# Kernel optimization log

Hardware: AMD Instinct MI355X
Metric: run time of the kernel (lower is better)

Reference implementation:

```python
import jax, jax.numpy as jnp
import numpy as np

N_ATOMS = 50000
N_EDGES = 1_600_000
N_MOL = 500
HIDDEN = 128
FILTERS = 128
GAUSS = 50
LAYERS = 3
CUTOFF = 10.0
LOG2 = 0.6931471805599453


def ssp(x):
    # ShiftedSoftplus: softplus(x) - log(2)
    return jax.nn.softplus(x) - LOG2


def setup_inputs() -> dict:
    key = jax.random.key(0)
    ks = jax.random.split(key, 24)
    z = jax.random.randint(ks[0], (N_ATOMS,), 0, 100)
    pos = jax.random.uniform(ks[1], (N_ATOMS, 3), jnp.float32) * 5.0  # box keeps d < cutoff
    batch = jnp.sort(jax.random.randint(ks[2], (N_ATOMS,), 0, N_MOL))
    row = jax.random.randint(ks[3], (N_EDGES,), 0, N_ATOMS)
    off = jax.random.randint(ks[4], (N_EDGES,), 1, N_ATOMS)
    col = (row + off) % N_ATOMS  # guarantees row != col (no zero distances)
    edge_index = jnp.stack([row, col])
    def lin(k, fi, fo):
        return jax.random.normal(k, (fi, fo), jnp.float32) * (1.0 / np.sqrt(fi))
    emb = jax.random.normal(ks[5], (100, HIDDEN), jnp.float32)
    mlp1_w = jnp.stack([lin(jax.random.fold_in(ks[6], i), GAUSS, FILTERS) for i in range(LAYERS)])
    mlp1_b = jnp.zeros((LAYERS, FILTERS), jnp.float32)
    mlp2_w = jnp.stack([lin(jax.random.fold_in(ks[7], i), FILTERS, FILTERS) for i in range(LAYERS)])
    mlp2_b = jnp.zeros((LAYERS, FILTERS), jnp.float32)
    lin1_w = jnp.stack([lin(jax.random.fold_in(ks[8], i), HIDDEN, FILTERS) for i in range(LAYERS)])
    lin2_w = jnp.stack([lin(jax.random.fold_in(ks[9], i), FILTERS, HIDDEN) for i in range(LAYERS)])
    lin2_b = jnp.zeros((LAYERS, HIDDEN), jnp.float32)
    int_w = jnp.stack([lin(jax.random.fold_in(ks[10], i), HIDDEN, HIDDEN) for i in range(LAYERS)])
    int_b = jnp.zeros((LAYERS, HIDDEN), jnp.float32)
    out1_w = lin(ks[11], HIDDEN, HIDDEN // 2)
    out1_b = jnp.zeros((HIDDEN // 2,), jnp.float32)
    out2_w = lin(ks[12], HIDDEN // 2, 1)
    out2_b = jnp.zeros((1,), jnp.float32)
    return {"z": z, "pos": pos, "batch": batch, "edge_index": edge_index,
            "emb": emb, "mlp1_w": mlp1_w, "mlp1_b": mlp1_b, "mlp2_w": mlp2_w, "mlp2_b": mlp2_b,
            "lin1_w": lin1_w, "lin2_w": lin2_w, "lin2_b": lin2_b, "int_w": int_w, "int_b": int_b,
            "out1_w": out1_w, "out1_b": out1_b, "out2_w": out2_w, "out2_b": out2_b}


def reference(z, pos, batch, edge_index, emb, mlp1_w, mlp1_b, mlp2_w, mlp2_b,
              lin1_w, lin2_w, lin2_b, int_w, int_b, out1_w, out1_b, out2_w, out2_b):
    row, col = edge_index[0], edge_index[1]  # source j, target i
    d = jnp.linalg.norm(pos[row] - pos[col], axis=-1)  # [E]
    # GaussianSmearing
    offset = jnp.linspace(0.0, CUTOFF, GAUSS)
    coeff = -0.5 / (offset[1] - offset[0]) ** 2
    rbf = jnp.exp(coeff * (d[:, None] - offset[None, :]) ** 2)  # [E, GAUSS]
    # cosine cutoff
    C = 0.5 * (jnp.cos(d * jnp.pi / CUTOFF) + 1.0)  # [E]
    h = emb[z]  # [N, H]
    for l in range(LAYERS):
        W = ssp(rbf @ mlp1_w[l] + mlp1_b[l]) @ mlp2_w[l] + mlp2_b[l]  # [E, F]
        W = W * C[:, None]
        x = h @ lin1_w[l]                 # [N, F]
        msg = x[row] * W                  # gather from source, per-edge filter
        agg = jax.ops.segment_sum(msg, col, num_segments=N_ATOMS)  # scatter-add to targets
        x = agg @ lin2_w[l] + lin2_b[l]
        x = ssp(x)
        x = x @ int_w[l] + int_b[l]
        h = h + x                         # residual
    h = ssp(h @ out1_w + out1_b)
    h = h @ out2_w + out2_b               # [N, 1] per-atom energy
    out = jax.ops.segment_sum(h[:, 0], batch, num_segments=N_MOL)  # 'add' readout
    return out.reshape(-1)
```

## Files before the change

kernel.cpp:

```cpp
#include <hip/hip_runtime.h>
#include <math.h>

#define HID 128
#define NGAUSS 50
#define TBL 2048
#define TBL2 8192
#define DMAX 8.6605f
#define LDX 136

typedef _Float16 h4 __attribute__((ext_vector_type(4)));
typedef _Float16 f16x8 __attribute__((ext_vector_type(8)));
typedef float f32x4 __attribute__((ext_vector_type(4)));

__device__ __forceinline__ float sspf(float x) {
  float ax = fabsf(x);
  return fmaxf(x, 0.0f) + log1pf(expf(-ax)) - 0.69314718055994530942f;
}

__global__ __launch_bounds__(128) void build_table_k(
    const float* __restrict__ w1, const float* __restrict__ b1,
    const float* __restrict__ w2, const float* __restrict__ b2,
    float* __restrict__ tab) {
  int l = blockIdx.x >> 11;
  int ti = blockIdx.x & (TBL - 1);
  int j = threadIdx.x;
  __shared__ float rbf[NGAUSS];
  __shared__ float v1[HID];
  const float step = DMAX / (float)(TBL - 1);
  float d = ti * step;
  if (j < NGAUSS) {
    const float gstep = 10.0f / 49.0f;
    const float gcoeff = -12.005f;
    float diff = d - j * gstep;
    rbf[j] = expf(gcoeff * diff * diff);
  }
  __syncthreads();
  float s = b1[l * HID + j];
  const float* w1p = w1 + l * NGAUSS * HID + j;
  for (int g = 0; g < NGAUSS; g++) s = fmaf(rbf[g], w1p[g * HID], s);
  v1[j] = sspf(s);
  __syncthreads();
  float s2 = b2[l * HID + j];
  const float* w2p = w2 + l * HID * HID + j;
  for (int k = 0; k < HID; k++) s2 = fmaf(v1[k], w2p[k * HID], s2);
  float C = 0.5f * (cosf(d * 0.3141592653589793f) + 1.0f);
  tab[((size_t)l * TBL + ti) * HID + j] = s2 * C;
}

__global__ __launch_bounds__(256) void upsample_k(
    const float* __restrict__ tab, _Float16* __restrict__ tabh) {
  int idx = blockIdx.x * 256 + threadIdx.x;
  if (idx >= 3 * TBL2 * HID) return;
  int ch = idx & 127;
  int i = (idx >> 7) & (TBL2 - 1);
  int l = idx >> 20;
  float t = (float)i * ((float)(TBL - 1) / (float)(TBL2 - 1));
  int i0 = min((int)t, TBL - 2);
  float f = t - (float)i0;
  const float* base = tab + ((size_t)l * TBL + i0) * HID + ch;
  tabh[idx] = (_Float16)fmaf(f, base[HID] - base[0], base[0]);
}

__global__ __launch_bounds__(256) void wtrans10_k(
    const float* __restrict__ lin1, const float* __restrict__ lin2,
    const float* __restrict__ intw, const float* __restrict__ out1w,
    _Float16* __restrict__ out) {
  int b = blockIdx.x;
  __shared__ _Float16 tile[128 * 130];
  int t = threadIdx.x;
  if (b < 9) {
    const float* src = (b < 3 ? lin1 : (b < 6 ? lin2 : intw)) + (size_t)(b % 3) * HID * HID;
    _Float16* dst = out + (size_t)b * HID * HID;
    for (int i = t; i < HID * HID; i += 256) tile[(i >> 7) * 130 + (i & 127)] = (_Float16)src[i];
    __syncthreads();
    for (int i = t; i < HID * HID; i += 256) dst[i] = tile[(i & 127) * 130 + (i >> 7)];
  } else {
    _Float16* dst = out + (size_t)9 * HID * HID;
    for (int i = t; i < 128 * 64; i += 256) tile[(i >> 6) * 66 + (i & 63)] = (_Float16)out1w[i];
    __syncthreads();
    for (int i = t; i < 64 * 128; i += 256) dst[i] = tile[(i & 127) * 66 + (i >> 7)];
  }
}

__global__ __launch_bounds__(256) void bcount_k(
    const int* __restrict__ col, int* __restrict__ bcount, int E, int nbuck) {
  __shared__ int hist[1024];
  int t = threadIdx.x;
  int e0 = blockIdx.x * 2048;
  for (int j = t; j < nbuck; j += 256) hist[j] = 0;
  __syncthreads();
#pragma unroll
  for (int u = 0; u < 8; u++) {
    int e = e0 + u * 256 + t;
    if (e < E) atomicAdd(&hist[col[e] >> 6], 1);
  }
  __syncthreads();
  for (int j = t; j < nbuck; j += 256)
    if (hist[j]) atomicAdd(&bcount[j], hist[j]);
}

__global__ __launch_bounds__(256) void bucket_scan_k(
    const int* __restrict__ bcount, int* __restrict__ bstart,
    int* __restrict__ bcur, int nbuck, int* __restrict__ starts, int N) {
  __shared__ int sh[256];
  int t = threadIdx.x;
  int chunk = (nbuck + 255) / 256;
  int b0 = t * chunk;
  int c[8];
  int s = 0;
  for (int j = 0; j < chunk; j++) {
    int idx = b0 + j;
    int v = (idx < nbuck) ? bcount[idx] : 0;
    c[j] = v;
    s += v;
  }
  sh[t] = s;
  __syncthreads();
  for (int o = 1; o < 256; o <<= 1) {
    int v = (t >= o) ? sh[t - o] : 0;
    __syncthreads();
    sh[t] += v;
    __syncthreads();
  }
  int p = (t == 0) ? 0 : sh[t - 1];
  for (int j = 0; j < chunk; j++) {
    int idx = b0 + j;
    if (idx < nbuck) {
      bstart[idx] = p;
      bcur[idx] = p;
      p += c[j];
    }
  }
  if (t == 255) {
    bstart[nbuck] = p;
    starts[N] = p;
  }
}

__global__ __launch_bounds__(256) void scatterA_k(
    const int* __restrict__ row, const int* __restrict__ col,
    const float* __restrict__ pos, int* __restrict__ bcur,
    unsigned long long* __restrict__ tmp, int E, int nbuck) {
  __shared__ int hist[1024];
  __shared__ int base[1024];
  int t = threadIdx.x;
  int e0 = blockIdx.x * 2048;
  for (int j = t; j < nbuck; j += 256) hist[j] = 0;
  __syncthreads();
  int bkt[8];
  int rnk[8];
  unsigned long long key[8];
#pragma unroll
  for (int u = 0; u < 8; u++) {
    int e = e0 + u * 256 + t;
    bkt[u] = -1;
    if (e < E) {
      int r = row[e], c = col[e];
      float dx = pos[r * 3 + 0] - pos[c * 3 + 0];
      float dy = pos[r * 3 + 1] - pos[c * 3 + 1];
      float dz = pos[r * 3 + 2] - pos[c * 3 + 2];
      float d = sqrtf(dx * dx + dy * dy + dz * dz);
      const float inv2 = (float)(TBL2 - 1) / DMAX;
      int q = min((int)(d * inv2 + 0.5f), TBL2 - 1);
      unsigned int pay = ((unsigned int)r << 13) | (unsigned int)q;
      key[u] = ((unsigned long long)pay << 6) | (unsigned long long)(c & 63);
      bkt[u] = c >> 6;
      rnk[u] = atomicAdd(&hist[bkt[u]], 1);
    }
  }
  __syncthreads();
  for (int j = t; j < nbuck; j += 256)
    base[j] = hist[j] ? atomicAdd(&bcur[j], hist[j]) : 0;
  __syncthreads();
#pragma unroll
  for (int u = 0; u < 8; u++)
    if (bkt[u] >= 0) tmp[(size_t)base[bkt[u]] + rnk[u]] = key[u];
}

__global__ __launch_bounds__(256) void scatterB_k(
    const unsigned long long* __restrict__ tmp, const int* __restrict__ bstart,
    int* __restrict__ starts, unsigned int* __restrict__ payload, int N) {
  int j = blockIdx.x;
  int t = threadIdx.x;
  __shared__ int cnt[64];
  __shared__ int cur[64];
  int rs = bstart[j], re = bstart[j + 1];
  if (t < 64) cnt[t] = 0;
  __syncthreads();
  for (int e = rs + t; e < re; e += 256)
    atomicAdd(&cnt[(int)(tmp[e] & 63)], 1);
  __syncthreads();
  if (t < 64) {
    int mine = cnt[t];
    int v = mine;
    for (int o = 1; o < 64; o <<= 1) {
      int u = __shfl_up(v, o, 64);
      if (t >= o) v += u;
    }
    int excl = v - mine;
    int c = j * 64 + t;
    if (c < N) starts[c] = rs + excl;
    cur[t] = rs + excl;
  }
  __syncthreads();
  for (int e = rs + t; e < re; e += 256) {
    unsigned long long k = tmp[e];
    int p = atomicAdd(&cur[(int)(k & 63)], 1);
    payload[p] = (unsigned int)(k >> 6);
  }
}

__global__ __launch_bounds__(256) void lin1_emb_k(
    const int* __restrict__ z, const float* __restrict__ emb,
    const _Float16* __restrict__ W1t, float* __restrict__ h,
    _Float16* __restrict__ x16, int N) {
  int t = threadIdx.x;
  int lane = t & 63, w = t >> 6;
  int mrow = lane & 15, quad = lane >> 4;
  int a0 = blockIdx.x * 64;
  int am = a0 + w * 16 + mrow;
  int amc = min(am, N - 1);
  int zz = z[amc];
  const float* er = emb + (size_t)zz * HID;
  f16x8 af[4];
#pragma unroll
  for (int kk = 0; kk < 4; kk++) {
    float4 e0 = *(const float4*)(er + kk * 32 + quad * 8);
    float4 e1 = *(const float4*)(er + kk * 32 + quad * 8 + 4);
    if (am < N) {
      *(float4*)(h + (size_t)am * HID + kk * 32 + quad * 8) = e0;
      *(float4*)(h + (size_t)am * HID + kk * 32 + quad * 8 + 4) = e1;
    }
    f16x8 a8;
    a8[0] = (_Float16)e0.x; a8[1] = (_Float16)e0.y;
    a8[2] = (_Float16)e0.z; a8[3] = (_Float16)e0.w;
    a8[4] = (_Float16)e1.x; a8[5] = (_Float16)e1.y;
    a8[6] = (_Float16)e1.z; a8[7] = (_Float16)e1.w;
    af[kk] = a8;
  }
  f32x4 zero = {0.f, 0.f, 0.f, 0.f};
  f32x4 acc[8];
#pragma unroll
  for (int i = 0; i < 8; i++) acc[i] = zero;
#pragma unroll
  for (int kk = 0; kk < 4; kk++) {
    f16x8 bf[8];
#pragma unroll
    for (int nt = 0; nt < 8; nt++)
      bf[nt] = *(const f16x8*)(W1t + (size_t)(nt * 16 + mrow) * HID + kk * 32 + quad * 8);
#pragma unroll
    for (int nt = 0; nt < 8; nt++)
      acc[nt] = __builtin_amdgcn_mfma_f32_16x16x32_f16(af[kk], bf[nt], acc[nt], 0, 0, 0);
  }
#pragma unroll
  for (int nt = 0; nt < 8; nt++) {
    int colv = nt * 16 + mrow;
#pragma unroll
    for (int r = 0; r < 4; r++) {
      int a = a0 + w * 16 + quad * 4 + r;
      if (a < N) x16[(size_t)a * HID + colv] = (_Float16)acc[nt][r];
    }
  }
}

__global__ __launch_bounds__(256) void fused_mid_k(
    const _Float16* __restrict__ agg16, const _Float16* __restrict__ W2t,
    const float* __restrict__ b2, const _Float16* __restrict__ W3t,
    const float* __restrict__ b3, float* __restrict__ h,
    const _Float16* __restrict__ W1nt, _Float16* __restrict__ x16, int N) {
  __shared__ __align__(16) _Float16 Xs[64 * LDX];
  int t = threadIdx.x;
  int lane = t & 63, w = t >> 6;
  int mrow = lane & 15, quad = lane >> 4;
  int a0 = blockIdx.x * 64;
  int am = min(a0 + w * 16 + mrow, N - 1);
  f16x8 af[4];
  const _Float16* arow = agg16 + (size_t)am * HID;
#pragma unroll
  for (int kk = 0; kk < 4; kk++)
    af[kk] = *(const f16x8*)(arow + kk * 32 + quad * 8);
  f32x4 zero = {0.f, 0.f, 0.f, 0.f};
  f32x4 acc[8];
#pragma unroll
  for (int i = 0; i < 8; i++) acc[i] = zero;
#pragma unroll
  for (int kk = 0; kk < 4; kk++) {
    f16x8 bf[8];
#pragma unroll
    for (int nt = 0; nt < 8; nt++)
      bf[nt] = *(const f16x8*)(W2t + (size_t)(nt * 16 + mrow) * HID + kk * 32 + quad * 8);
#pragma unroll
    for (int nt = 0; nt < 8; nt++)
      acc[nt] = __builtin_amdgcn_mfma_f32_16x16x32_f16(af[kk], bf[nt], acc[nt], 0, 0, 0);
  }
#pragma unroll
  for (int nt = 0; nt < 8; nt++) {
    float bb = b2[nt * 16 + mrow];
#pragma unroll
    for (int r = 0; r < 4; r++)
      Xs[(w * 16 + quad * 4 + r) * LDX + nt * 16 + mrow] = (_Float16)sspf(acc[nt][r] + bb);
  }
#pragma unroll
  for (int kk = 0; kk < 4; kk++)
    af[kk] = *(const f16x8*)&Xs[(w * 16 + mrow) * LDX + kk * 32 + quad * 8];
#pragma unroll
  for (int i = 0; i < 8; i++) acc[i] = zero;
#pragma unroll
  for (int kk = 0; kk < 4; kk++) {
    f16x8 bf[8];
#pragma unroll
    for (int nt = 0; nt < 8; nt++)
      bf[nt] = *(const f16x8*)(W3t + (size_t)(nt * 16 + mrow) * HID + kk * 32 + quad * 8);
#pragma unroll
    for (int nt = 0; nt < 8; nt++)
      acc[nt] = __builtin_amdgcn_mfma_f32_16x16x32_f16(af[kk], bf[nt], acc[nt], 0, 0, 0);
  }
#pragma unroll
  for (int nt = 0; nt < 8; nt++) {
    int colv = nt * 16 + mrow;
    float bb = b3[colv];
#pragma unroll
    for (int r = 0; r < 4; r++) {
      int a = a0 + w * 16 + quad * 4 + r;
      float v = acc[nt][r] + bb;
      if (a < N) {
        float* hp = h + (size_t)a * HID + colv;
        v += *hp;
        *hp = v;
      }
      Xs[(w * 16 + quad * 4 + r) * LDX + colv] = (_Float16)v;
    }
  }
#pragma unroll
  for (int kk = 0; kk < 4; kk++)
    af[kk] = *(const f16x8*)&Xs[(w * 16 + mrow) * LDX + kk * 32 + quad * 8];
#pragma unroll
  for (int i = 0; i < 8; i++) acc[i] = zero;
#pragma unroll
  for (int kk = 0; kk < 4; kk++) {
    f16x8 bf[8];
#pragma unroll
    for (int nt = 0; nt < 8; nt++)
      bf[nt] = *(const f16x8*)(W1nt + (size_t)(nt * 16 + mrow) * HID + kk * 32 + quad * 8);
#pragma unroll
    for (int nt = 0; nt < 8; nt++)
      acc[nt] = __builtin_amdgcn_mfma_f32_16x16x32_f16(af[kk], bf[nt], acc[nt], 0, 0, 0);
  }
#pragma unroll
  for (int nt = 0; nt < 8; nt++) {
    int colv = nt * 16 + mrow;
#pragma unroll
    for (int r = 0; r < 4; r++) {
      int a = a0 + w * 16 + quad * 4 + r;
      if (a < N) x16[(size_t)a * HID + colv] = (_Float16)acc[nt][r];
    }
  }
}

__global__ __launch_bounds__(256) void fused_last_k(
    const _Float16* __restrict__ agg16, const _Float16* __restrict__ W2t,
    const float* __restrict__ b2, const _Float16* __restrict__ W3t,
    const float* __restrict__ b3, const float* __restrict__ h,
    const _Float16* __restrict__ Wo1t, const float* __restrict__ o1b,
    const float* __restrict__ o2w, const float* __restrict__ o2b,
    const int* __restrict__ batch, float* __restrict__ out, int N) {
  __shared__ __align__(16) _Float16 Xs[64 * LDX];
  int t = threadIdx.x;
  int lane = t & 63, w = t >> 6;
  int mrow = lane & 15, quad = lane >> 4;
  int a0 = blockIdx.x * 64;
  int am = min(a0 + w * 16 + mrow, N - 1);
  f16x8 af[4];
  const _Float16* arow = agg16 + (size_t)am * HID;
#pragma unroll
  for (int kk = 0; kk < 4; kk++)
    af[kk] = *(const f16x8*)(arow + kk * 32 + quad * 8);
  f32x4 zero = {0.f, 0.f, 0.f, 0.f};
  f32x4 acc[8];
#pragma unroll
  for (int i = 0; i < 8; i++) acc[i] = zero;
#pragma unroll
  for (int kk = 0; kk < 4; kk++) {
    f16x8 bf[8];
#pragma unroll
    for (int nt = 0; nt < 8; nt++)
      bf[nt] = *(const f16x8*)(W2t + (size_t)(nt * 16 + mrow) * HID + kk * 32 + quad * 8);
#pragma unroll
    for (int nt = 0; nt < 8; nt++)
      acc[nt] = __builtin_amdgcn_mfma_f32_16x16x32_f16(af[kk], bf[nt], acc[nt], 0, 0, 0);
  }
#pragma unroll
  for (int nt = 0; nt < 8; nt++) {
    float bb = b2[nt * 16 + mrow];
#pragma unroll
    for (int r = 0; r < 4; r++)
      Xs[(w * 16 + quad * 4 + r) * LDX + nt * 16 + mrow] = (_Float16)sspf(acc[nt][r] + bb);
  }
#pragma unroll
  for (int kk = 0; kk < 4; kk++)
    af[kk] = *(const f16x8*)&Xs[(w * 16 + mrow) * LDX + kk * 32 + quad * 8];
#pragma unroll
  for (int i = 0; i < 8; i++) acc[i] = zero;
#pragma unroll
  for (int kk = 0; kk < 4; kk++) {
    f16x8 bf[8];
#pragma unroll
    for (int nt = 0; nt < 8; nt++)
      bf[nt] = *(const f16x8*)(W3t + (size_t)(nt * 16 + mrow) * HID + kk * 32 + quad * 8);
#pragma unroll
    for (int nt = 0; nt < 8; nt++)
      acc[nt] = __builtin_amdgcn_mfma_f32_16x16x32_f16(af[kk], bf[nt], acc[nt], 0, 0, 0);
  }
#pragma unroll
  for (int nt = 0; nt < 8; nt++) {
    int colv = nt * 16 + mrow;
    float bb = b3[colv];
#pragma unroll
    for (int r = 0; r < 4; r++) {
      int a = a0 + w * 16 + quad * 4 + r;
      float v = acc[nt][r] + bb;
      if (a < N) v += h[(size_t)a * HID + colv];
      Xs[(w * 16 + quad * 4 + r) * LDX + colv] = (_Float16)v;
    }
  }
#pragma unroll
  for (int kk = 0; kk < 4; kk++)
    af[kk] = *(const f16x8*)&Xs[(w * 16 + mrow) * LDX + kk * 32 + quad * 8];
#pragma unroll
  for (int i = 0; i < 4; i++) acc[i] = zero;
#pragma unroll
  for (int kk = 0; kk < 4; kk++) {
    f16x8 bf[4];
#pragma unroll
    for (int nt = 0; nt < 4; nt++)
      bf[nt] = *(const f16x8*)(Wo1t + (size_t)(nt * 16 + mrow) * HID + kk * 32 + quad * 8);
#pragma unroll
    for (int nt = 0; nt < 4; nt++)
      acc[nt] = __builtin_amdgcn_mfma_f32_16x16x32_f16(af[kk], bf[nt], acc[nt], 0, 0, 0);
  }
  float o2b0 = o2b[0];
  float ss[4] = {0.f, 0.f, 0.f, 0.f};
#pragma unroll
  for (int nt = 0; nt < 4; nt++) {
    float bb = o1b[nt * 16 + mrow];
    float ww = o2w[nt * 16 + mrow];
#pragma unroll
    for (int r = 0; r < 4; r++) ss[r] += sspf(acc[nt][r] + bb) * ww;
  }
#pragma unroll
  for (int r = 0; r < 4; r++) {
    ss[r] += __shfl_xor(ss[r], 1);
    ss[r] += __shfl_xor(ss[r], 2);
    ss[r] += __shfl_xor(ss[r], 4);
    ss[r] += __shfl_xor(ss[r], 8);
    int a = a0 + w * 16 + quad * 4 + r;
    if (mrow == 0 && a < N) atomicAdd(&out[batch[a]], ss[r] + o2b0);
  }
}

__global__ __launch_bounds__(256) void aggregate_k(
    const int* __restrict__ starts, const unsigned int* __restrict__ payload,
    const _Float16* __restrict__ x16, const _Float16* __restrict__ tabh,
    _Float16* __restrict__ agg16, int N) {
  int a = blockIdx.x * 4 + (threadIdx.x >> 6);
  if (a >= N) return;
  int lane = threadIdx.x & 63;
  int half = lane >> 5;
  int sl = lane & 31;
  int s = starts[a], e_end = starts[a + 1];
  float4 acc0 = make_float4(0.f, 0.f, 0.f, 0.f);
  float4 acc1 = make_float4(0.f, 0.f, 0.f, 0.f);
  auto do_edge = [&](unsigned int p, float4& acc) {
    int tq = (int)(p & 8191u);
    int r = (int)(p >> 13);
    h4 tw = *(const h4*)&tabh[(size_t)tq * HID + sl * 4];
    h4 xr = *(const h4*)&x16[(size_t)r * HID + sl * 4];
    acc.x = fmaf((float)xr.x, (float)tw.x, acc.x);
    acc.y = fmaf((float)xr.y, (float)tw.y, acc.y);
    acc.z = fmaf((float)xr.z, (float)tw.z, acc.z);
    acc.w = fmaf((float)xr.w, (float)tw.w, acc.w);
  };
  int i = s;
  for (; i + 8 <= e_end; i += 8) {
    unsigned int p0 = payload[i + half];
    unsigned int p1 = payload[i + 2 + half];
    unsigned int p2 = payload[i + 4 + half];
    unsigned int p3 = payload[i + 6 + half];
    do_edge(p0, acc0);
    do_edge(p1, acc1);
    do_edge(p2, acc0);
    do_edge(p3, acc1);
  }
  for (; i < e_end; i += 2) {
    int e = i + half;
    if (e < e_end) do_edge(payload[e], acc0);
  }
  acc0.x += acc1.x; acc0.y += acc1.y; acc0.z += acc1.z; acc0.w += acc1.w;
  acc0.x += __shfl_xor(acc0.x, 32);
  acc0.y += __shfl_xor(acc0.y, 32);
  acc0.z += __shfl_xor(acc0.z, 32);
  acc0.w += __shfl_xor(acc0.w, 32);
  if (half == 0) {
    h4 o;
    o.x = (_Float16)acc0.x; o.y = (_Float16)acc0.y;
    o.z = (_Float16)acc0.z; o.w = (_Float16)acc0.w;
    *(h4*)&agg16[(size_t)a * HID + sl * 4] = o;
  }
}

extern "C" void kernel_launch(void* const* d_in, const int* in_sizes, int n_in,
                              void* d_out, int out_size, void* d_ws, size_t ws_size,
                              hipStream_t stream) {
  const int* z = (const int*)d_in[0];
  const float* pos = (const float*)d_in[1];
  const int* batch = (const int*)d_in[2];
  const int* eidx = (const int*)d_in[3];
  const float* emb = (const float*)d_in[4];
  const float* mlp1_w = (const float*)d_in[5];
  const float* mlp1_b = (const float*)d_in[6];
  const float* mlp2_w = (const float*)d_in[7];
  const float* mlp2_b = (const float*)d_in[8];
  const float* lin1_w = (const float*)d_in[9];
  const float* lin2_w = (const float*)d_in[10];
  const float* lin2_b = (const float*)d_in[11];
  const float* int_w = (const float*)d_in[12];
  const float* int_b = (const float*)d_in[13];
  const float* out1_w = (const float*)d_in[14];
  const float* out1_b = (const float*)d_in[15];
  const float* out2_w = (const float*)d_in[16];
  const float* out2_b = (const float*)d_in[17];
  float* out = (float*)d_out;

  const int N = in_sizes[0];
  const int E = in_sizes[3] / 2;
  const int* row = eidx;
  const int* col = eidx + E;
  const int nbuck = (N + 63) / 64;

  char* ws = (char*)d_ws;
  size_t off = 0;
  auto alloc = [&](size_t bytes) -> void* {
    void* p = ws + off;
    off = (off + bytes + 255) & ~(size_t)255;
    return p;
  };
  float* h = (float*)alloc((size_t)N * HID * 4);
  _Float16* x16 = (_Float16*)alloc((size_t)N * HID * 2);
  size_t agg_bytes = (size_t)N * HID * 2;
  size_t tmp_bytes = (size_t)E * 8 + 16;
  void* agg_union = alloc(agg_bytes > tmp_bytes ? agg_bytes : tmp_bytes);
  _Float16* agg16 = (_Float16*)agg_union;
  unsigned long long* tmp = (unsigned long long*)agg_union;
  unsigned int* payload = (unsigned int*)alloc((size_t)E * 4 + 16);
  int* starts = (int*)alloc((size_t)(N + 1) * 4);
  int* bcount = (int*)alloc((size_t)nbuck * 4);
  int* bstart = (int*)alloc((size_t)(nbuck + 1) * 4);
  int* bcur = (int*)alloc((size_t)nbuck * 4);
  float* tab = (float*)alloc((size_t)3 * TBL * HID * 4);
  _Float16* tabh = (_Float16*)alloc((size_t)3 * TBL2 * HID * 2);
  _Float16* Wt10 = (_Float16*)alloc((size_t)10 * HID * HID * 2);
  (void)ws_size;

  hipMemsetAsync(bcount, 0, (size_t)nbuck * 4, stream);
  hipMemsetAsync(out, 0, (size_t)out_size * 4, stream);

  build_table_k<<<3 * TBL, 128, 0, stream>>>(mlp1_w, mlp1_b, mlp2_w, mlp2_b, tab);
  upsample_k<<<(3 * TBL2 * HID + 255) / 256, 256, 0, stream>>>(tab, tabh);
  wtrans10_k<<<10, 256, 0, stream>>>(lin1_w, lin2_w, int_w, out1_w, Wt10);
  bcount_k<<<(E + 2047) / 2048, 256, 0, stream>>>(col, bcount, E, nbuck);
  bucket_scan_k<<<1, 256, 0, stream>>>(bcount, bstart, bcur, nbuck, starts, N);
  scatterA_k<<<(E + 2047) / 2048, 256, 0, stream>>>(row, col, pos, bcur, tmp, E, nbuck);
  scatterB_k<<<nbuck, 256, 0, stream>>>(tmp, bstart, starts, payload, N);

  int gemm_grid = (N + 63) / 64;
  lin1_emb_k<<<gemm_grid, 256, 0, stream>>>(z, emb, Wt10, h, x16, N);
  for (int l = 0; l < 2; l++) {
    aggregate_k<<<(N + 3) / 4, 256, 0, stream>>>(starts, payload, x16,
                                                 tabh + (size_t)l * TBL2 * HID, agg16, N);
    fused_mid_k<<<gemm_grid, 256, 0, stream>>>(
        agg16, Wt10 + (size_t)(3 + l) * HID * HID, lin2_b + (size_t)l * HID,
        Wt10 + (size_t)(6 + l) * HID * HID, int_b + (size_t)l * HID, h,
        Wt10 + (size_t)(l + 1) * HID * HID, x16, N);
  }
  aggregate_k<<<(N + 3) / 4, 256, 0, stream>>>(starts, payload, x16,
                                               tabh + (size_t)2 * TBL2 * HID, agg16, N);
  fused_last_k<<<gemm_grid, 256, 0, stream>>>(
      agg16, Wt10 + (size_t)5 * HID * HID, lin2_b + (size_t)2 * HID,
      Wt10 + (size_t)8 * HID * HID, int_b + (size_t)2 * HID, h,
      Wt10 + (size_t)9 * HID * HID, out1_b, out2_w, out2_b, batch, out, N);
}
```

Before: 658.2 us.

## Retile node GEMM kernels to 32 atoms per block with staged coalesced I/O

The per-atom GEMM kernels (embedding+lin1, fused mid layers, fused last layer) now handle 32 atoms per block instead of 64. The four waves are split as 2 row groups by 2 column halves, so each wave keeps 4 accumulator tiles instead of 8 and the grid has twice as many blocks. Global loads and stores of agg16, h and x16 are staged through shared memory so they are coalesced vector accesses, replacing scattered per-element writes. The final readout first sums per-atom energies in shared memory before issuing global atomics. The cost is extra __syncthreads, extra LDS traffic, and each weight matrix being read by twice as many blocks.

```diff
diff --git a/kernel.cpp b/kernel.cpp
--- a/kernel.cpp
+++ b/kernel.cpp
@@ -210,56 +210,65 @@
   }
 }
 
+
 __global__ __launch_bounds__(256) void lin1_emb_k(
     const int* __restrict__ z, const float* __restrict__ emb,
     const _Float16* __restrict__ W1t, float* __restrict__ h,
     _Float16* __restrict__ x16, int N) {
+  __shared__ __align__(16) _Float16 Xs[32 * LDX];
+  __shared__ __align__(16) _Float16 Ys[32 * LDX];
+  __shared__ int zi[32];
   int t = threadIdx.x;
   int lane = t & 63, w = t >> 6;
+  int g = w & 1, c = w >> 1;
   int mrow = lane & 15, quad = lane >> 4;
-  int a0 = blockIdx.x * 64;
-  int am = a0 + w * 16 + mrow;
-  int amc = min(am, N - 1);
-  int zz = z[amc];
-  const float* er = emb + (size_t)zz * HID;
+  int a0 = blockIdx.x * 32;
+  if (t < 32) zi[t] = (a0 + t < N) ? z[a0 + t] : 0;
+  __syncthreads();
+#pragma unroll
+  for (int p = 0; p < 4; p++) {
+    int id = t + p * 256;
+    int a = id >> 5, kg = id & 31;
+    float4 v = ((const float4*)emb)[(size_t)zi[a] * 32 + kg];
+    if (a0 + a < N) ((float4*)h)[(size_t)(a0 + a) * 32 + kg] = v;
+    h4 o;
+    o.x = (_Float16)v.x; o.y = (_Float16)v.y;
+    o.z = (_Float16)v.z; o.w = (_Float16)v.w;
+    *(h4*)&Xs[a * LDX + kg * 4] = o;
+  }
+  __syncthreads();
   f16x8 af[4];
 #pragma unroll
+  for (int kk = 0; kk < 4; kk++)
+    af[kk] = *(const f16x8*)&Xs[(g * 16 + mrow) * LDX + kk * 32 + quad * 8];
+  f32x4 zero = {0.f, 0.f, 0.f, 0.f};
+  f32x4 acc[4];
+#pragma unroll
+  for (int i = 0; i < 4; i++) acc[i] = zero;
+#pragma unroll
   for (int kk = 0; kk < 4; kk++) {
-    float4 e0 = *(const float4*)(er + kk * 32 + quad * 8);
-    float4 e1 = *(const float4*)(er + kk * 32 + quad * 8 + 4);
-    if (am < N) {
-      *(float4*)(h + (size_t)am * HID + kk * 32 + quad * 8) = e0;
-      *(float4*)(h + (size_t)am * HID + kk * 32 + quad * 8 + 4) = e1;
-    }
-    f16x8 a8;
-    a8[0] = (_Float16)e0.x; a8[1] = (_Float16)e0.y;
-    a8[2] = (_Float16)e0.z; a8[3] = (_Float16)e0.w;
-    a8[4] = (_Float16)e1.x; a8[5] = (_Float16)e1.y;
-    a8[6] = (_Float16)e1.z; a8[7] = (_Float16)e1.w;
-    af[kk] = a8;
-  }
-  f32x4 zero = {0.f, 0.f, 0.f, 0.f};
-  f32x4 acc[8];
-#pragma unroll
-  for (int i = 0; i < 8; i++) acc[i] = zero;
-#pragma unroll
-  for (int kk = 0; kk < 4; kk++) {
-    f16x8 bf[8];
-#pragma unroll
-    for (int nt = 0; nt < 8; nt++)
-      bf[nt] = *(const f16x8*)(W1t + (size_t)(nt * 16 + mrow) * HID + kk * 32 + quad * 8);
-#pragma unroll
-    for (int nt = 0; nt < 8; nt++)
+    f16x8 bf[4];
+#pragma unroll
+    for (int nt = 0; nt < 4; nt++)
+      bf[nt] = *(const f16x8*)(W1t + (size_t)(c * 64 + nt * 16 + mrow) * HID + kk * 32 + quad * 8);
+#pragma unroll
+    for (int nt = 0; nt < 4; nt++)
       acc[nt] = __builtin_amdgcn_mfma_f32_16x16x32_f16(af[kk], bf[nt], acc[nt], 0, 0, 0);
   }
 #pragma unroll
-  for (int nt = 0; nt < 8; nt++) {
-    int colv = nt * 16 + mrow;
-#pragma unroll
-    for (int r = 0; r < 4; r++) {
-      int a = a0 + w * 16 + quad * 4 + r;
-      if (a < N) x16[(size_t)a * HID + colv] = (_Float16)acc[nt][r];
-    }
+  for (int nt = 0; nt < 4; nt++) {
+    int colv = c * 64 + nt * 16 + mrow;
+#pragma unroll
+    for (int r = 0; r < 4; r++)
+      Ys[(g * 16 + quad * 4 + r) * LDX + colv] = (_Float16)acc[nt][r];
+  }
+  __syncthreads();
+#pragma unroll
+  for (int p = 0; p < 2; p++) {
+    int id = t + p * 256;
+    int a = id >> 4, kg = id & 15;
+    if (a0 + a < N)
+      ((uint4*)x16)[(size_t)(a0 + a) * 16 + kg] = *(uint4*)&Ys[a * LDX + kg * 8];
   }
 }
 
@@ -268,92 +277,119 @@
     const float* __restrict__ b2, const _Float16* __restrict__ W3t,
     const float* __restrict__ b3, float* __restrict__ h,
     const _Float16* __restrict__ W1nt, _Float16* __restrict__ x16, int N) {
-  __shared__ __align__(16) _Float16 Xs[64 * LDX];
+  __shared__ __align__(16) _Float16 Xs[32 * LDX];
+  __shared__ __align__(16) _Float16 Ys[32 * LDX];
   int t = threadIdx.x;
   int lane = t & 63, w = t >> 6;
+  int g = w & 1, c = w >> 1;
   int mrow = lane & 15, quad = lane >> 4;
-  int a0 = blockIdx.x * 64;
-  int am = min(a0 + w * 16 + mrow, N - 1);
+  int a0 = blockIdx.x * 32;
+#pragma unroll
+  for (int p = 0; p < 2; p++) {
+    int id = t + p * 256;
+    int a = id >> 4, kg = id & 15;
+    uint4 v = make_uint4(0, 0, 0, 0);
+    if (a0 + a < N) v = ((const uint4*)agg16)[(size_t)(a0 + a) * 16 + kg];
+    *(uint4*)&Xs[a * LDX + kg * 8] = v;
+  }
+  __syncthreads();
+  f32x4 zero = {0.f, 0.f, 0.f, 0.f};
   f16x8 af[4];
-  const _Float16* arow = agg16 + (size_t)am * HID;
+  f32x4 acc[4];
 #pragma unroll
   for (int kk = 0; kk < 4; kk++)
-    af[kk] = *(const f16x8*)(arow + kk * 32 + quad * 8);
-  f32x4 zero = {0.f, 0.f, 0.f, 0.f};
-  f32x4 acc[8];
-#pragma unroll
-  for (int i = 0; i < 8; i++) acc[i] = zero;
+    af[kk] = *(const f16x8*)&Xs[(g * 16 + mrow) * LDX + kk * 32 + quad * 8];
+#pragma unroll
+  for (int i = 0; i < 4; i++) acc[i] = zero;
 #pragma unroll
   for (int kk = 0; kk < 4; kk++) {
-    f16x8 bf[8];
-#pragma unroll
-    for (int nt = 0; nt < 8; nt++)
-      bf[nt] = *(const f16x8*)(W2t + (size_t)(nt * 16 + mrow) * HID + kk * 32 + quad * 8);
-#pragma unroll
-    for (int nt = 0; nt < 8; nt++)
+    f16x8 bf[4];
+#pragma unroll
+    for (int nt = 0; nt < 4; nt++)
+      bf[nt] = *(const f16x8*)(W2t + (size_t)(c * 64 + nt * 16 + mrow) * HID + kk * 32 + quad * 8);
+#pragma unroll
+    for (int nt = 0; nt < 4; nt++)
       acc[nt] = __builtin_amdgcn_mfma_f32_16x16x32_f16(af[kk], bf[nt], acc[nt], 0, 0, 0);
   }
 #pragma unroll
-  for (int nt = 0; nt < 8; nt++) {
-    float bb = b2[nt * 16 + mrow];
+  for (int nt = 0; nt < 4; nt++) {
+    int colv = c * 64 + nt * 16 + mrow;
+    float bb = b2[colv];
 #pragma unroll
     for (int r = 0; r < 4; r++)
-      Xs[(w * 16 + quad * 4 + r) * LDX + nt * 16 + mrow] = (_Float16)sspf(acc[nt][r] + bb);
-  }
+      Ys[(g * 16 + quad * 4 + r) * LDX + colv] = (_Float16)sspf(acc[nt][r] + bb);
+  }
+  __syncthreads();
 #pragma unroll
   for (int kk = 0; kk < 4; kk++)
-    af[kk] = *(const f16x8*)&Xs[(w * 16 + mrow) * LDX + kk * 32 + quad * 8];
-#pragma unroll
-  for (int i = 0; i < 8; i++) acc[i] = zero;
+    af[kk] = *(const f16x8*)&Ys[(g * 16 + mrow) * LDX + kk * 32 + quad * 8];
+#pragma unroll
+  for (int i = 0; i < 4; i++) acc[i] = zero;
 #pragma unroll
   for (int kk = 0; kk < 4; kk++) {
-    f16x8 bf[8];
-#pragma unroll
-    for (int nt = 0; nt < 8; nt++)
-      bf[nt] = *(const f16x8*)(W3t + (size_t)(nt * 16 + mrow) * HID + kk * 32 + quad * 8);
-#pragma unroll
-    for (int nt = 0; nt < 8; nt++)
+    f16x8 bf[4];
+#pragma unroll
+    for (int nt = 0; nt < 4; nt++)
+      bf[nt] = *(const f16x8*)(W3t + (size_t)(c * 64 + nt * 16 + mrow) * HID + kk * 32 + quad * 8);
+#pragma unroll
+    for (int nt = 0; nt < 4; nt++)
       acc[nt] = __builtin_amdgcn_mfma_f32_16x16x32_f16(af[kk], bf[nt], acc[nt], 0, 0, 0);
   }
 #pragma unroll
-  for (int nt = 0; nt < 8; nt++) {
-    int colv = nt * 16 + mrow;
+  for (int nt = 0; nt < 4; nt++) {
+    int colv = c * 64 + nt * 16 + mrow;
     float bb = b3[colv];
 #pragma unroll
-    for (int r = 0; r < 4; r++) {
-      int a = a0 + w * 16 + quad * 4 + r;
-      float v = acc[nt][r] + bb;
-      if (a < N) {
-        float* hp = h + (size_t)a * HID + colv;
-        v += *hp;
-        *hp = v;
-      }
-      Xs[(w * 16 + quad * 4 + r) * LDX + colv] = (_Float16)v;
+    for (int r = 0; r < 4; r++)
+      Xs[(g * 16 + quad * 4 + r) * LDX + colv] = (_Float16)(acc[nt][r] + bb);
+  }
+  __syncthreads();
+#pragma unroll
+  for (int p = 0; p < 4; p++) {
+    int id = t + p * 256;
+    int a = id >> 5, kg = id & 31;
+    h4 xv = *(h4*)&Xs[a * LDX + kg * 4];
+    float4 v = make_float4((float)xv.x, (float)xv.y, (float)xv.z, (float)xv.w);
+    if (a0 + a < N) {
+      float4 ho = ((const float4*)h)[(size_t)(a0 + a) * 32 + kg];
+      v.x += ho.x; v.y += ho.y; v.z += ho.z; v.w += ho.w;
+      ((float4*)h)[(size_t)(a0 + a) * 32 + kg] = v;
     }
-  }
+    h4 o;
+    o.x = (_Float16)v.x; o.y = (_Float16)v.y;
+    o.z = (_Float16)v.z; o.w = (_Float16)v.w;
+    *(h4*)&Xs[a * LDX + kg * 4] = o;
+  }
+  __syncthreads();
 #pragma unroll
   for (int kk = 0; kk < 4; kk++)
-    af[kk] = *(const f16x8*)&Xs[(w * 16 + mrow) * LDX + kk * 32 + quad * 8];
-#pragma unroll
-  for (int i = 0; i < 8; i++) acc[i] = zero;
+    af[kk] = *(const f16x8*)&Xs[(g * 16 + mrow) * LDX + kk * 32 + quad * 8];
+#pragma unroll
+  for (int i = 0; i < 4; i++) acc[i] = zero;
 #pragma unroll
   for (int kk = 0; kk < 4; kk++) {
-    f16x8 bf[8];
-#pragma unroll
-    for (int nt = 0; nt < 8; nt++)
-      bf[nt] = *(const f16x8*)(W1nt + (size_t)(nt * 16 + mrow) * HID + kk * 32 + quad * 8);
-#pragma unroll
-    for (int nt = 0; nt < 8; nt++)
+    f16x8 bf[4];
+#pragma unroll
+    for (int nt = 0; nt < 4; nt++)
+      bf[nt] = *(const f16x8*)(W1nt + (size_t)(c * 64 + nt * 16 + mrow) * HID + kk * 32 + quad * 8);
+#pragma unroll
+    for (int nt = 0; nt < 4; nt++)
       acc[nt] = __builtin_amdgcn_mfma_f32_16x16x32_f16(af[kk], bf[nt], acc[nt], 0, 0, 0);
   }
 #pragma unroll
-  for (int nt = 0; nt < 8; nt++) {
-    int colv = nt * 16 + mrow;
-#pragma unroll
-    for (int r = 0; r < 4; r++) {
-      int a = a0 + w * 16 + quad * 4 + r;
-      if (a < N) x16[(size_t)a * HID + colv] = (_Float16)acc[nt][r];
-    }
+  for (int nt = 0; nt < 4; nt++) {
+    int colv = c * 64 + nt * 16 + mrow;
+#pragma unroll
+    for (int r = 0; r < 4; r++)
+      Ys[(g * 16 + quad * 4 + r) * LDX + colv] = (_Float16)acc[nt][r];
+  }
+  __syncthreads();
+#pragma unroll
+  for (int p = 0; p < 2; p++) {
+    int id = t + p * 256;
+    int a = id >> 4, kg = id & 15;
+    if (a0 + a < N)
+      ((uint4*)x16)[(size_t)(a0 + a) * 16 + kg] = *(uint4*)&Ys[a * LDX + kg * 8];
   }
 }
 
@@ -364,68 +400,30 @@
     const _Float16* __restrict__ Wo1t, const float* __restrict__ o1b,
     const float* __restrict__ o2w, const float* __restrict__ o2b,
     const int* __restrict__ batch, float* __restrict__ out, int N) {
-  __shared__ __align__(16) _Float16 Xs[64 * LDX];
+  __shared__ __align__(16) _Float16 Xs[32 * LDX];
+  __shared__ __align__(16) _Float16 Ys[32 * LDX];
+  __shared__ float ebuf[32];
   int t = threadIdx.x;
   int lane = t & 63, w = t >> 6;
+  int g = w & 1, c = w >> 1;
   int mrow = lane & 15, quad = lane >> 4;
-  int a0 = blockIdx.x * 64;
-  int am = min(a0 + w * 16 + mrow, N - 1);
+  int a0 = blockIdx.x * 32;
+  if (t < 32) ebuf[t] = 0.f;
+#pragma unroll
+  for (int p = 0; p < 2; p++) {
+    int id = t + p * 256;
+    int a = id >> 4, kg = id & 15;
+    uint4 v = make_uint4(0, 0, 0, 0);
+    if (a0 + a < N) v = ((const uint4*)agg16)[(size_t)(a0 + a) * 16 + kg];
+    *(uint4*)&Xs[a * LDX + kg * 8] = v;
+  }
+  __syncthreads();
+  f32x4 zero = {0.f, 0.f, 0.f, 0.f};
   f16x8 af[4];
-  const _Float16* arow = agg16 + (size_t)am * HID;
+  f32x4 acc[4];
 #pragma unroll
   for (int kk = 0; kk < 4; kk++)
-    af[kk] = *(const f16x8*)(arow + kk * 32 + quad * 8);
-  f32x4 zero = {0.f, 0.f, 0.f, 0.f};
-  f32x4 acc[8];
-#pragma unroll
-  for (int i = 0; i < 8; i++) acc[i] = zero;
-#pragma unroll
-  for (int kk = 0; kk < 4; kk++) {
-    f16x8 bf[8];
-#pragma unroll
-    for (int nt = 0; nt < 8; nt++)
-      bf[nt] = *(const f16x8*)(W2t + (size_t)(nt * 16 + mrow) * HID + kk * 32 + quad * 8);
-#pragma unroll
-    for (int nt = 0; nt < 8; nt++)
-      acc[nt] = __builtin_amdgcn_mfma_f32_16x16x32_f16(af[kk], bf[nt], acc[nt], 0, 0, 0);
-  }
-#pragma unroll
-  for (int nt = 0; nt < 8; nt++) {
-    float bb = b2[nt * 16 + mrow];
-#pragma unroll
-    for (int r = 0; r < 4; r++)
-      Xs[(w * 16 + quad * 4 + r) * LDX + nt * 16 + mrow] = (_Float16)sspf(acc[nt][r] + bb);
-  }
-#pragma unroll
-  for (int kk = 0; kk < 4; kk++)
-    af[kk] = *(const f16x8*)&Xs[(w * 16 + mrow) * LDX + kk * 32 + quad * 8];
-#pragma unroll
-  for (int i = 0; i < 8; i++) acc[i] = zero;
-#pragma unroll
-  for (int kk = 0; kk < 4; kk++) {
-    f16x8 bf[8];
-#pragma unroll
-    for (int nt = 0; nt < 8; nt++)
-      bf[nt] = *(const f16x8*)(W3t + (size_t)(nt * 16 + mrow) * HID + kk * 32 + quad * 8);
-#pragma unroll
-    for (int nt = 0; nt < 8; nt++)
-      acc[nt] = __builtin_amdgcn_mfma_f32_16x16x32_f16(af[kk], bf[nt], acc[nt], 0, 0, 0);
-  }
-#pragma unroll
-  for (int nt = 0; nt < 8; nt++) {
-    int colv = nt * 16 + mrow;
-    float bb = b3[colv];
-#pragma unroll
-    for (int r = 0; r < 4; r++) {
-      int a = a0 + w * 16 + quad * 4 + r;
-      float v = acc[nt][r] + bb;
-      if (a < N) v += h[(size_t)a * HID + colv];
-      Xs[(w * 16 + quad * 4 + r) * LDX + colv] = (_Float16)v;
-    }
-  }
-#pragma unroll
-  for (int kk = 0; kk < 4; kk++)
-    af[kk] = *(const f16x8*)&Xs[(w * 16 + mrow) * LDX + kk * 32 + quad * 8];
+    af[kk] = *(const f16x8*)&Xs[(g * 16 + mrow) * LDX + kk * 32 + quad * 8];
 #pragma unroll
   for (int i = 0; i < 4; i++) acc[i] = zero;
 #pragma unroll
@@ -433,17 +431,81 @@
     f16x8 bf[4];
 #pragma unroll
     for (int nt = 0; nt < 4; nt++)
-      bf[nt] = *(const f16x8*)(Wo1t + (size_t)(nt * 16 + mrow) * HID + kk * 32 + quad * 8);
+      bf[nt] = *(const f16x8*)(W2t + (size_t)(c * 64 + nt * 16 + mrow) * HID + kk * 32 + quad * 8);
 #pragma unroll
     for (int nt = 0; nt < 4; nt++)
       acc[nt] = __builtin_amdgcn_mfma_f32_16x16x32_f16(af[kk], bf[nt], acc[nt], 0, 0, 0);
   }
-  float o2b0 = o2b[0];
+#pragma unroll
+  for (int nt = 0; nt < 4; nt++) {
+    int colv = c * 64 + nt * 16 + mrow;
+    float bb = b2[colv];
+#pragma unroll
+    for (int r = 0; r < 4; r++)
+      Ys[(g * 16 + quad * 4 + r) * LDX + colv] = (_Float16)sspf(acc[nt][r] + bb);
+  }
+  __syncthreads();
+#pragma unroll
+  for (int kk = 0; kk < 4; kk++)
+    af[kk] = *(const f16x8*)&Ys[(g * 16 + mrow) * LDX + kk * 32 + quad * 8];
+#pragma unroll
+  for (int i = 0; i < 4; i++) acc[i] = zero;
+#pragma unroll
+  for (int kk = 0; kk < 4; kk++) {
+    f16x8 bf[4];
+#pragma unroll
+    for (int nt = 0; nt < 4; nt++)
+      bf[nt] = *(const f16x8*)(W3t + (size_t)(c * 64 + nt * 16 + mrow) * HID + kk * 32 + quad * 8);
+#pragma unroll
+    for (int nt = 0; nt < 4; nt++)
+      acc[nt] = __builtin_amdgcn_mfma_f32_16x16x32_f16(af[kk], bf[nt], acc[nt], 0, 0, 0);
+  }
+#pragma unroll
+  for (int nt = 0; nt < 4; nt++) {
+    int colv = c * 64 + nt * 16 + mrow;
+    float bb = b3[colv];
+#pragma unroll
+    for (int r = 0; r < 4; r++)
+      Xs[(g * 16 + quad * 4 + r) * LDX + colv] = (_Float16)(acc[nt][r] + bb);
+  }
+  __syncthreads();
+#pragma unroll
+  for (int p = 0; p < 4; p++) {
+    int id = t + p * 256;
+    int a = id >> 5, kg = id & 31;
+    h4 xv = *(h4*)&Xs[a * LDX + kg * 4];
+    float4 v = make_float4((float)xv.x, (float)xv.y, (float)xv.z, (float)xv.w);
+    if (a0 + a < N) {
+      float4 ho = ((const float4*)h)[(size_t)(a0 + a) * 32 + kg];
+      v.x += ho.x; v.y += ho.y; v.z += ho.z; v.w += ho.w;
+    }
+    h4 o;
+    o.x = (_Float16)v.x; o.y = (_Float16)v.y;
+    o.z = (_Float16)v.z; o.w = (_Float16)v.w;
+    *(h4*)&Xs[a * LDX + kg * 4] = o;
+  }
+  __syncthreads();
+#pragma unroll
+  for (int kk = 0; kk < 4; kk++)
+    af[kk] = *(const f16x8*)&Xs[(g * 16 + mrow) * LDX + kk * 32 + quad * 8];
+#pragma unroll
+  for (int i = 0; i < 2; i++) acc[i] = zero;
+#pragma unroll
+  for (int kk = 0; kk < 4; kk++) {
+    f16x8 bf[2];
+#pragma unroll
+    for (int nt = 0; nt < 2; nt++)
+      bf[nt] = *(const f16x8*)(Wo1t + (size_t)(c * 32 + nt * 16 + mrow) * HID + kk * 32 + quad * 8);
+#pragma unroll
+    for (int nt = 0; nt < 2; nt++)
+      acc[nt] = __builtin_amdgcn_mfma_f32_16x16x32_f16(af[kk], bf[nt], acc[nt], 0, 0, 0);
+  }
   float ss[4] = {0.f, 0.f, 0.f, 0.f};
 #pragma unroll
-  for (int nt = 0; nt < 4; nt++) {
-    float bb = o1b[nt * 16 + mrow];
-    float ww = o2w[nt * 16 + mrow];
+  for (int nt = 0; nt < 2; nt++) {
+    int colv = c * 32 + nt * 16 + mrow;
+    float bb = o1b[colv];
+    float ww = o2w[colv];
 #pragma unroll
     for (int r = 0; r < 4; r++) ss[r] += sspf(acc[nt][r] + bb) * ww;
   }
@@ -453,8 +515,12 @@
     ss[r] += __shfl_xor(ss[r], 2);
     ss[r] += __shfl_xor(ss[r], 4);
     ss[r] += __shfl_xor(ss[r], 8);
-    int a = a0 + w * 16 + quad * 4 + r;
-    if (mrow == 0 && a < N) atomicAdd(&out[batch[a]], ss[r] + o2b0);
+    if (mrow == 0) atomicAdd(&ebuf[g * 16 + quad * 4 + r], ss[r]);
+  }
+  __syncthreads();
+  if (t < 32) {
+    int a = a0 + t;
+    if (a < N) atomicAdd(&out[batch[a]], ebuf[t] + o2b[0]);
   }
 }
 
@@ -572,19 +638,19 @@
   scatterA_k<<<(E + 2047) / 2048, 256, 0, stream>>>(row, col, pos, bcur, tmp, E, nbuck);
   scatterB_k<<<nbuck, 256, 0, stream>>>(tmp, bstart, starts, payload, N);
 
-  int gemm_grid = (N + 63) / 64;
-  lin1_emb_k<<<gemm_grid, 256, 0, stream>>>(z, emb, Wt10, h, x16, N);
+  int g32 = (N + 31) / 32;
+  lin1_emb_k<<<g32, 256, 0, stream>>>(z, emb, Wt10, h, x16, N);
   for (int l = 0; l < 2; l++) {
     aggregate_k<<<(N + 3) / 4, 256, 0, stream>>>(starts, payload, x16,
                                                  tabh + (size_t)l * TBL2 * HID, agg16, N);
-    fused_mid_k<<<gemm_grid, 256, 0, stream>>>(
+    fused_mid_k<<<g32, 256, 0, stream>>>(
         agg16, Wt10 + (size_t)(3 + l) * HID * HID, lin2_b + (size_t)l * HID,
         Wt10 + (size_t)(6 + l) * HID * HID, int_b + (size_t)l * HID, h,
         Wt10 + (size_t)(l + 1) * HID * HID, x16, N);
   }
   aggregate_k<<<(N + 3) / 4, 256, 0, stream>>>(starts, payload, x16,
                                                tabh + (size_t)2 * TBL2 * HID, agg16, N);
-  fused_last_k<<<gemm_grid, 256, 0, stream>>>(
+  fused_last_k<<<g32, 256, 0, stream>>>(
       agg16, Wt10 + (size_t)5 * HID * HID, lin2_b + (size_t)2 * HID,
       Wt10 + (size_t)8 * HID * HID, int_b + (size_t)2 * HID, h,
       Wt10 + (size_t)9 * HID * HID, out1_b, out2_w, out2_b, batch, out, N);
```

Result: faster. 617.5 us (-6.2%).
